# Optimization experiments

Measured on AMD Instinct MI355X. Metric: run time of the kernel, lower is better.

## Reference

```python
import jax, jax.numpy as jnp
import numpy as np

N = 4096
F_IN = 512
F_OUT = 64
H = 8
ALPHA = 0.2
NEG_BIG = -9e15


def setup_inputs() -> dict:
    key = jax.random.key(0)
    ks = jax.random.split(key, 7)
    h = jax.random.normal(ks[0], (N, F_IN), dtype=jnp.float32)
    mask = jax.random.randint(ks[1], (N, N), 0, 2, dtype=jnp.int32)
    # per-head linear W: weight [H, F_IN, F_OUT], bias [H, F_OUT] (xavier-ish scale)
    w_scale = 1.414 * np.sqrt(6.0 / (F_IN + F_OUT))
    W = jax.random.uniform(ks[2], (H, F_IN, F_OUT), dtype=jnp.float32, minval=-w_scale, maxval=w_scale)
    bW = jnp.zeros((H, F_OUT), dtype=jnp.float32)
    # attention linear A: [2*F_OUT, 1] split into a_l (acts on Wh_i) and a_r (acts on Wh_j)
    a_scale = 1.414 * np.sqrt(6.0 / (2 * F_OUT + 1))
    a_l = jax.random.uniform(ks[3], (H, F_OUT), dtype=jnp.float32, minval=-a_scale, maxval=a_scale)
    a_r = jax.random.uniform(ks[4], (H, F_OUT), dtype=jnp.float32, minval=-a_scale, maxval=a_scale)
    bA = jnp.zeros((H,), dtype=jnp.float32)
    return {"h": h, "mask": mask, "W": W, "bW": bW, "a_l": a_l, "a_r": a_r, "bA": bA}


def reference(h, mask, W, bW, a_l, a_r, bA):
    # Wh: [H, N, F_OUT]
    Wh = jnp.einsum('ni,hio->hno', h, W) + bW[:, None, :]
    # A([Wh_i ; Wh_j]) decomposed as outer sum: e[h,i,j] = a_l.Wh_i + a_r.Wh_j + bA
    el = jnp.einsum('hno,ho->hn', Wh, a_l)  # [H, N]
    er = jnp.einsum('hno,ho->hn', Wh, a_r)  # [H, N]
    e = el[:, :, None] + er[:, None, :] + bA[:, None, None]  # [H, N, N]
    e = jax.nn.leaky_relu(e, negative_slope=ALPHA)
    e = jnp.where(mask[None] > 0, e, NEG_BIG)
    a = jax.nn.softmax(e, axis=-1)  # softmax over neighbors j (dim=1 in torch)
    # dropout omitted (eval mode / deterministic reference)
    aWh = jnp.einsum('hij,hjo->hio', a, Wh)  # [H, N, F_OUT]
    out = jax.nn.elu(aWh)  # last=False
    # concat heads along feature dim -> [N, H*F_OUT]
    return jnp.transpose(out, (1, 0, 2)).reshape(N, H * F_OUT)
```

## Files before the change

### kernel.cpp

```cpp
#include <hip/hip_runtime.h>
#include <hip/hip_bf16.h>

#define NN 4096
#define FIN 512
#define FOUT 64
#define NH 8
#define ALPHA 0.2f

typedef unsigned int uint;
typedef unsigned short ushort;
typedef unsigned char uchar;
typedef unsigned long long ull;
typedef __attribute__((ext_vector_type(8))) short short8;
typedef __attribute__((ext_vector_type(4))) float floatx4;

__device__ __forceinline__ float bf2f(ushort s) { return __uint_as_float(((uint)s) << 16); }
__device__ __forceinline__ ushort f2bf(float f) {
    uint u = __float_as_uint(f);
    u += 0x7fffu + ((u >> 16) & 1u);
    return (ushort)(u >> 16);
}

__device__ __forceinline__ int detect_bf16(const ushort* __restrict__ hraw) {
    int lane = threadIdx.x & 63;
    float a = fabsf(bf2f(hraw[2 * lane]));
    ull bal = __ballot(a >= 1e-3f && a <= 100.0f);
    return __popcll(bal) >= 32;
}

#define PM_BLKS 8192
#define CV_BLKS 1024
#define TW_BLKS 32

__global__ __launch_bounds__(256) void prep_kernel(
    const int* __restrict__ mask, uchar* __restrict__ mb,
    const void* __restrict__ hraw, ushort* __restrict__ bh,
    const void* __restrict__ Wraw, ushort* __restrict__ WT)
{
    const int b = blockIdx.x, t = threadIdx.x;
    if (b < PM_BLKS) {
        size_t gid = (size_t)b * 256 + t;
        const int* p = mask + gid * 8;
        int4 aa = *(const int4*)p;
        int4 bb = *(const int4*)(p + 4);
        uint by = (uint)(aa.x > 0)        | ((uint)(aa.y > 0) << 1)
                | ((uint)(aa.z > 0) << 2) | ((uint)(aa.w > 0) << 3)
                | ((uint)(bb.x > 0) << 4) | ((uint)(bb.y > 0) << 5)
                | ((uint)(bb.z > 0) << 6) | ((uint)(bb.w > 0) << 7);
        mb[gid] = (uchar)by;
    } else if (b < PM_BLKS + CV_BLKS) {
        int isbf = detect_bf16((const ushort*)hraw);
        size_t e0 = ((size_t)(b - PM_BLKS) * 256 + t) * 8;
        if (isbf) {
            *(uint4*)(bh + e0) = *(const uint4*)((const ushort*)hraw + e0);
        } else {
            const float* s = (const float*)hraw + e0;
            float4 f0 = *(const float4*)s;
            float4 f1 = *(const float4*)(s + 4);
            uint4 o;
            o.x = (uint)f2bf(f0.x) | ((uint)f2bf(f0.y) << 16);
            o.y = (uint)f2bf(f0.z) | ((uint)f2bf(f0.w) << 16);
            o.z = (uint)f2bf(f1.x) | ((uint)f2bf(f1.y) << 16);
            o.w = (uint)f2bf(f1.z) | ((uint)f2bf(f1.w) << 16);
            *(uint4*)(bh + e0) = o;
        }
    } else {
        int isbf = detect_bf16((const ushort*)hraw);
        int b2 = b - PM_BLKS - CV_BLKS;
        int h = b2 >> 2, kq = b2 & 3;
        int o = t & 63, sub = t >> 6;
        int kbase = kq * 128 + sub * 32;
        uint pk[16];
#pragma unroll
        for (int kk = 0; kk < 32; kk += 2) {
            float v0, v1;
            size_t s0 = ((size_t)h * FIN + kbase + kk) * FOUT + o;
            size_t s1 = s0 + FOUT;
            if (isbf) { v0 = bf2f(((const ushort*)Wraw)[s0]); v1 = bf2f(((const ushort*)Wraw)[s1]); }
            else      { v0 = ((const float*)Wraw)[s0];        v1 = ((const float*)Wraw)[s1]; }
            pk[kk >> 1] = (uint)f2bf(v0) | ((uint)f2bf(v1) << 16);
        }
        ushort* dst = WT + ((size_t)h * FOUT + o) * FIN + kbase;
#pragma unroll
        for (int q = 0; q < 4; q++)
            *(uint4*)(dst + q * 8) = make_uint4(pk[q*4], pk[q*4+1], pk[q*4+2], pk[q*4+3]);
    }
}

__global__ __launch_bounds__(256) void khv_kernel(const float* __restrict__ er,
                                                  float* __restrict__ Kh,
                                                  float* __restrict__ vt,
                                                  float* __restrict__ zt) {
    __shared__ float red[256];
    int h = blockIdx.x >> 3, sl = blockIdx.x & 7, t = threadIdx.x;
    float m = -3.0e38f;
    for (int j = t; j < NN; j += 256) m = fmaxf(m, er[(size_t)h * NN + j]);
    red[t] = m;
    __syncthreads();
    for (int s = 128; s >= 1; s >>= 1) {
        if (t < s) red[t] = fmaxf(red[t], red[t + s]);
        __syncthreads();
    }
    float kh = red[0];
    if (t == 0 && sl == 0) Kh[h] = kh;
    int j = sl * 512 + t;
#pragma unroll
    for (int q = 0; q < 2; q++, j += 256) {
        float d = er[(size_t)h * NN + j] - kh;
        vt[(size_t)h * NN + j] = __expf(d);
        zt[(size_t)h * NN + j] = __expf(ALPHA * d);
    }
}

__global__ __launch_bounds__(256) void wh_kernel(
    const ushort* __restrict__ hmat, const ushort* __restrict__ WT,
    const void* __restrict__ bWr, const void* __restrict__ alr,
    const void* __restrict__ arr, const void* __restrict__ bAr,
    const ushort* __restrict__ hraw,
    ushort* __restrict__ WhT, float* __restrict__ el, float* __restrict__ er)
{
    __shared__ __align__(16) ushort sT[64][72];
    const int t = threadIdx.x, lane = t & 63, wid = t >> 6;
    const int head = blockIdx.y, rbase = blockIdx.x * 64;
    const int lm = lane & 15, lq = lane >> 4;

    floatx4 C[4];
#pragma unroll
    for (int cg = 0; cg < 4; cg++) C[cg] = (floatx4){0.f, 0.f, 0.f, 0.f};

    const ushort* Ap = hmat + (size_t)(rbase + wid * 16 + lm) * FIN + lq * 8;
    const ushort* Bp = WT + (size_t)head * FOUT * FIN + (size_t)lm * FIN + lq * 8;

#pragma unroll
    for (int kc = 0; kc < 16; kc++) {
        short8 a = *(const short8*)(Ap + kc * 32);
#pragma unroll
        for (int cg = 0; cg < 4; cg++) {
            short8 b = *(const short8*)(Bp + (size_t)cg * 16 * FIN + kc * 32);
            C[cg] = __builtin_amdgcn_mfma_f32_16x16x32_bf16(a, b, C[cg], 0, 0, 0);
        }
    }

    const int isbf = detect_bf16(hraw);
    float bA = isbf ? bf2f(((const ushort*)bAr)[head]) : ((const float*)bAr)[head];
    float pel[4] = {0.f, 0.f, 0.f, 0.f}, per[4] = {0.f, 0.f, 0.f, 0.f};
#pragma unroll
    for (int cg = 0; cg < 4; cg++) {
        int o = head * FOUT + cg * 16 + lm;
        float bw = isbf ? bf2f(((const ushort*)bWr)[o]) : ((const float*)bWr)[o];
        float av = isbf ? bf2f(((const ushort*)alr)[o]) : ((const float*)alr)[o];
        float rv = isbf ? bf2f(((const ushort*)arr)[o]) : ((const float*)arr)[o];
        ushort pk[4];
#pragma unroll
        for (int r = 0; r < 4; r++) {
            float v = C[cg][r] + bw;
            pel[r] += v * av;
            per[r] += v * rv;
            pk[r] = f2bf(v);
        }
        ushort4 p4; p4.x = pk[0]; p4.y = pk[1]; p4.z = pk[2]; p4.w = pk[3];
        *(ushort4*)(&sT[cg * 16 + lm][wid * 16 + lq * 4]) = p4;
    }
#pragma unroll
    for (int off = 1; off < 16; off <<= 1) {
#pragma unroll
        for (int r = 0; r < 4; r++) {
            pel[r] += __shfl_xor(pel[r], off);
            per[r] += __shfl_xor(per[r], off);
        }
    }
    if (lm == 0) {
#pragma unroll
        for (int r = 0; r < 4; r++) {
            int row = rbase + wid * 16 + lq * 4 + r;
            el[(size_t)head * NN + row] = pel[r];
            er[(size_t)head * NN + row] = per[r] + bA;
        }
    }
    __syncthreads();
    {
        int o = t >> 2, ch = t & 3;
        uint4 v0 = *(const uint4*)(&sT[o][ch * 16]);
        uint4 v1 = *(const uint4*)(&sT[o][ch * 16 + 8]);
        ushort* d = WhT + ((size_t)head * FOUT + o) * NN + rbase + ch * 16;
        *(uint4*)d = v0;
        *(uint4*)(d + 8) = v1;
    }
}

__device__ __forceinline__ uint ppair(float v0, float v1, float z0, float z1,
                                      uint m2, float ui, float wi) {
    float p0 = fmaxf(ui * v0, wi * z0);
    float p1 = fmaxf(ui * v1, wi * z1);
    uint k0 = (uint)0 - (m2 & 1u);
    uint k1 = (uint)0 - ((m2 >> 1) & 1u);
    p0 = __uint_as_float(__float_as_uint(p0) & k0);
    p1 = __uint_as_float(__float_as_uint(p1) & k1);
    __hip_bfloat162 r = __float22bfloat162_rn(make_float2(p0, p1));
    return *(uint*)&r;
}

__device__ __forceinline__ short8 pgen8(float4 va, float4 vb, float4 za, float4 zb,
                                        uint mby, float ui, float wi) {
    union { uint4 u; short8 s; } c;
    c.u.x = ppair(va.x, va.y, za.x, za.y, mby,      ui, wi);
    c.u.y = ppair(va.z, va.w, za.z, za.w, mby >> 2, ui, wi);
    c.u.z = ppair(vb.x, vb.y, zb.x, zb.y, mby >> 4, ui, wi);
    c.u.w = ppair(vb.z, vb.w, zb.z, zb.w, mby >> 6, ui, wi);
    return c.s;
}

#define VZLOAD(S, j0) do {                                      \
    v##S##a = *(const float4*)(gvt + (j0) + sh8);               \
    v##S##b = *(const float4*)(gvt + (j0) + sh8 + 4);           \
    v##S##c = *(const float4*)(gvt + (j0) + 32 + sh8);          \
    v##S##d = *(const float4*)(gvt + (j0) + 32 + sh8 + 4);      \
    z##S##a = *(const float4*)(gzt + (j0) + sh8);               \
    z##S##b = *(const float4*)(gzt + (j0) + sh8 + 4);           \
    z##S##c = *(const float4*)(gzt + (j0) + 32 + sh8);          \
    z##S##d = *(const float4*)(gzt + (j0) + 32 + sh8 + 4);      \
} while (0)

__global__ __launch_bounds__(256, 2) void attn_kernel(
    const uchar* __restrict__ mb,
    const ushort* __restrict__ WhT,
    const float* __restrict__ el, const float* __restrict__ Kh,
    const float* __restrict__ vt, const float* __restrict__ zt,
    const ushort* __restrict__ hraw,
    void* __restrict__ outv)
{
    __shared__ __align__(16) ushort sB[2][64 * 72];

    const int t = threadIdx.x, lane = t & 63, wid = t >> 6;
    const int b = blockIdx.x;
    const int head = b & 7;
    const int ibase = (b >> 3) * 64;
    const int lm = lane & 15, lq = lane >> 4;
    const int sh8 = lq * 8;

    const float kh = Kh[head];
    const int row = ibase + wid * 16 + lm;
    const float x = el[(size_t)head * NN + row] + kh;
    const float Mi = fmaxf(x, ALPHA * x);
    const float ui = __expf(x - Mi);
    const float wi = __expf(ALPHA * x - Mi);

    const int so = t >> 2;
    const int sc = (t & 3) * 16;
    const ushort* gB = WhT + ((size_t)head * FOUT + so) * NN + sc;
    const float* gvt = vt + (size_t)head * NN;
    const float* gzt = zt + (size_t)head * NN;
    const uchar* mrow = mb + (size_t)row * 512;

    uint4 rr0, rr1;
    uint2 mk_s;

    auto gload = [&](int j0) {
        rr0 = *(const uint4*)(gB + j0);
        rr1 = *(const uint4*)(gB + j0 + 8);
        mk_s = *(const uint2*)(mrow + (j0 >> 3));
    };
    auto lwrite = [&](int buf) {
        ushort* d = &sB[buf][so * 72 + sc];
        *(uint4*)(d)     = rr0;
        *(uint4*)(d + 8) = rr1;
    };

    float4 v0a, v0b, v0c, v0d, z0a, z0b, z0c, z0d;
    float4 v1a, v1b, v1c, v1d, z1a, z1b, z1c, z1d;

    const short8 ones = {0x3F80, 0x3F80, 0x3F80, 0x3F80, 0x3F80, 0x3F80, 0x3F80, 0x3F80};
    floatx4 Z = {0.f, 0.f, 0.f, 0.f};
    floatx4 C0 = Z, C1 = Z, C2 = Z, C3 = Z, Cd = Z;

    auto compute = [&](int buf, uint2 mk,
                       float4 va, float4 vb, float4 vc, float4 vd,
                       float4 za, float4 zb, float4 zc, float4 zd) {
        uint m0 = (mk.x >> sh8) & 0xFFu;
        uint m1 = (mk.y >> sh8) & 0xFFu;
        short8 a0 = pgen8(va, vb, za, zb, m0, ui, wi);
        short8 a1 = pgen8(vc, vd, zc, zd, m1, ui, wi);
        const ushort* base = &sB[buf][0];
        short8 b00 = *(const short8*)(base + (0  + lm) * 72 + sh8);
        short8 b10 = *(const short8*)(base + (16 + lm) * 72 + sh8);
        short8 b20 = *(const short8*)(base + (32 + lm) * 72 + sh8);
        short8 b30 = *(const short8*)(base + (48 + lm) * 72 + sh8);
        Cd = __builtin_amdgcn_mfma_f32_16x16x32_bf16(a0, ones, Cd, 0, 0, 0);
        C0 = __builtin_amdgcn_mfma_f32_16x16x32_bf16(a0, b00, C0, 0, 0, 0);
        C1 = __builtin_amdgcn_mfma_f32_16x16x32_bf16(a0, b10, C1, 0, 0, 0);
        C2 = __builtin_amdgcn_mfma_f32_16x16x32_bf16(a0, b20, C2, 0, 0, 0);
        C3 = __builtin_amdgcn_mfma_f32_16x16x32_bf16(a0, b30, C3, 0, 0, 0);
        short8 b01 = *(const short8*)(base + (0  + lm) * 72 + 32 + sh8);
        short8 b11 = *(const short8*)(base + (16 + lm) * 72 + 32 + sh8);
        short8 b21 = *(const short8*)(base + (32 + lm) * 72 + 32 + sh8);
        short8 b31 = *(const short8*)(base + (48 + lm) * 72 + 32 + sh8);
        Cd = __builtin_amdgcn_mfma_f32_16x16x32_bf16(a1, ones, Cd, 0, 0, 0);
        C0 = __builtin_amdgcn_mfma_f32_16x16x32_bf16(a1, b01, C0, 0, 0, 0);
        C1 = __builtin_amdgcn_mfma_f32_16x16x32_bf16(a1, b11, C1, 0, 0, 0);
        C2 = __builtin_amdgcn_mfma_f32_16x16x32_bf16(a1, b21, C2, 0, 0, 0);
        C3 = __builtin_amdgcn_mfma_f32_16x16x32_bf16(a1, b31, C3, 0, 0, 0);
    };

    uint2 mk0, mk1;
    gload(0);
    lwrite(0);
    mk0 = mk_s;
    gload(64);
    VZLOAD(0, 0);
    __syncthreads();

    for (int it = 0; it < 64; it += 2) {
        lwrite(1);
        mk1 = mk_s;
        gload(((it + 2) & 63) * 64);
        VZLOAD(1, (it + 1) * 64);
        compute(0, mk0, v0a, v0b, v0c, v0d, z0a, z0b, z0c, z0d);
        __syncthreads();
        lwrite(0);
        mk0 = mk_s;
        gload(((it + 3) & 63) * 64);
        VZLOAD(0, ((it + 2) & 63) * 64);
        compute(1, mk1, v1a, v1b, v1c, v1d, z1a, z1b, z1c, z1d);
        __syncthreads();
    }

    const int isbf = detect_bf16(hraw);
#pragma unroll
    for (int r = 0; r < 4; r++) {
        int orow = ibase + wid * 16 + lq * 4 + r;
        float inv = 1.f / Cd[r];
        float x0 = C0[r] * inv; x0 = (x0 > 0.f) ? x0 : __expf(x0) - 1.f;
        float x1 = C1[r] * inv; x1 = (x1 > 0.f) ? x1 : __expf(x1) - 1.f;
        float x2 = C2[r] * inv; x2 = (x2 > 0.f) ? x2 : __expf(x2) - 1.f;
        float x3 = C3[r] * inv; x3 = (x3 > 0.f) ? x3 : __expf(x3) - 1.f;
        size_t base = (size_t)orow * (NH * FOUT) + head * FOUT + lm;
        if (isbf) {
            ushort* o = (ushort*)outv;
            o[base + 0]  = f2bf(x0);
            o[base + 16] = f2bf(x1);
            o[base + 32] = f2bf(x2);
            o[base + 48] = f2bf(x3);
        } else {
            float* o = (float*)outv;
            o[base + 0]  = x0;
            o[base + 16] = x1;
            o[base + 32] = x2;
            o[base + 48] = x3;
        }
    }
}

extern "C" void kernel_launch(void* const* d_in, const int* in_sizes, int n_in,
                              void* d_out, int out_size, void* d_ws, size_t ws_size,
                              hipStream_t stream)
{
    const void* hraw = d_in[0];
    const int*  mask = (const int*)d_in[1];
    const void* Wraw = d_in[2];
    const void* bWr  = d_in[3];
    const void* alr  = d_in[4];
    const void* arr  = d_in[5];
    const void* bAr  = d_in[6];

    char* w = (char*)d_ws;
    ushort* bh   = (ushort*)w;                  w += (size_t)NN * FIN * 2;
    ushort* WT   = (ushort*)w;                  w += (size_t)NH * FOUT * FIN * 2;
    ushort* WhT  = (ushort*)w;                  w += (size_t)NH * FOUT * NN * 2;
    float*  el   = (float*)w;                   w += (size_t)NH * NN * 4;
    float*  er   = (float*)w;                   w += (size_t)NH * NN * 4;
    float*  Kh   = (float*)w;                   w += 64;
    float*  vt   = (float*)w;                   w += (size_t)NH * NN * 4;
    float*  zt   = (float*)w;                   w += (size_t)NH * NN * 4;
    uchar*  mb   = (uchar*)w;                   w += (size_t)NN * 512;

    prep_kernel<<<PM_BLKS + CV_BLKS + TW_BLKS, 256, 0, stream>>>(
        mask, mb, hraw, bh, Wraw, WT);
    wh_kernel<<<dim3(NN / 64, NH), 256, 0, stream>>>(bh, WT, bWr, alr, arr, bAr,
                                                     (const ushort*)hraw, WhT, el, er);
    khv_kernel<<<64, 256, 0, stream>>>(er, Kh, vt, zt);
    attn_kernel<<<NN / 64 * NH, 256, 0, stream>>>(mb, WhT, el, Kh, vt, zt,
                                                  (const ushort*)hraw, d_out);
}
```

Measured before the change: 190.1 us.

## Split neighbor loop across two wave groups per block and reduce through LDS

The attention block grows to 512 threads made of two groups of four waves. Each group handles half of the neighbor range (j), using its own double-buffered LDS tile of Wh. At the end, group 1 writes its partial accumulators and softmax denominators to LDS, and group 0 adds them before normalizing and applying ELU. The aim is to double resident waves per CU and halve each wave's serial loop. In exchange it adds an LDS reduction step and tighter launch bounds, which may force fewer registers and cause spills.

```diff
diff --git a/kernel.cpp b/kernel.cpp
--- a/kernel.cpp
+++ b/kernel.cpp
@@ -221,7 +221,7 @@
     z##S##d = *(const float4*)(gzt + (j0) + 32 + sh8 + 4);      \
 } while (0)
 
-__global__ __launch_bounds__(256, 2) void attn_kernel(
+__global__ __launch_bounds__(512, 4) void attn_kernel(
     const uchar* __restrict__ mb,
     const ushort* __restrict__ WhT,
     const float* __restrict__ el, const float* __restrict__ Kh,
@@ -229,9 +229,11 @@
     const ushort* __restrict__ hraw,
     void* __restrict__ outv)
 {
-    __shared__ __align__(16) ushort sB[2][64 * 72];
+    __shared__ __align__(16) ushort sB[2][2][64 * 72];
 
     const int t = threadIdx.x, lane = t & 63, wid = t >> 6;
+    const int g  = wid >> 2;
+    const int wv = wid & 3;
     const int b = blockIdx.x;
     const int head = b & 7;
     const int ibase = (b >> 3) * 64;
@@ -239,18 +241,19 @@
     const int sh8 = lq * 8;
 
     const float kh = Kh[head];
-    const int row = ibase + wid * 16 + lm;
+    const int row = ibase + wv * 16 + lm;
     const float x = el[(size_t)head * NN + row] + kh;
     const float Mi = fmaxf(x, ALPHA * x);
     const float ui = __expf(x - Mi);
     const float wi = __expf(ALPHA * x - Mi);
 
-    const int so = t >> 2;
-    const int sc = (t & 3) * 16;
-    const ushort* gB = WhT + ((size_t)head * FOUT + so) * NN + sc;
-    const float* gvt = vt + (size_t)head * NN;
-    const float* gzt = zt + (size_t)head * NN;
-    const uchar* mrow = mb + (size_t)row * 512;
+    const int st = t & 255;
+    const int so = st >> 2;
+    const int sc = (st & 3) * 16;
+    const ushort* gB = WhT + ((size_t)head * FOUT + so) * NN + g * 2048 + sc;
+    const float* gvt = vt + (size_t)head * NN + g * 2048;
+    const float* gzt = zt + (size_t)head * NN + g * 2048;
+    const uchar* mrow = mb + (size_t)row * 512 + g * 256;
 
     uint4 rr0, rr1;
     uint2 mk_s;
@@ -261,7 +264,7 @@
         mk_s = *(const uint2*)(mrow + (j0 >> 3));
     };
     auto lwrite = [&](int buf) {
-        ushort* d = &sB[buf][so * 72 + sc];
+        ushort* d = &sB[g][buf][so * 72 + sc];
         *(uint4*)(d)     = rr0;
         *(uint4*)(d + 8) = rr1;
     };
@@ -280,7 +283,7 @@
         uint m1 = (mk.y >> sh8) & 0xFFu;
         short8 a0 = pgen8(va, vb, za, zb, m0, ui, wi);
         short8 a1 = pgen8(vc, vd, zc, zd, m1, ui, wi);
-        const ushort* base = &sB[buf][0];
+        const ushort* base = &sB[g][buf][0];
         short8 b00 = *(const short8*)(base + (0  + lm) * 72 + sh8);
         short8 b10 = *(const short8*)(base + (16 + lm) * 72 + sh8);
         short8 b20 = *(const short8*)(base + (32 + lm) * 72 + sh8);
@@ -309,43 +312,66 @@
     VZLOAD(0, 0);
     __syncthreads();
 
-    for (int it = 0; it < 64; it += 2) {
+    for (int it = 0; it < 32; it += 2) {
         lwrite(1);
         mk1 = mk_s;
-        gload(((it + 2) & 63) * 64);
+        gload(((it + 2) & 31) * 64);
         VZLOAD(1, (it + 1) * 64);
         compute(0, mk0, v0a, v0b, v0c, v0d, z0a, z0b, z0c, z0d);
         __syncthreads();
         lwrite(0);
         mk0 = mk_s;
-        gload(((it + 3) & 63) * 64);
-        VZLOAD(0, ((it + 2) & 63) * 64);
+        gload(((it + 3) & 31) * 64);
+        VZLOAD(0, ((it + 2) & 31) * 64);
         compute(1, mk1, v1a, v1b, v1c, v1d, z1a, z1b, z1c, z1d);
         __syncthreads();
     }
 
-    const int isbf = detect_bf16(hraw);
-#pragma unroll
-    for (int r = 0; r < 4; r++) {
-        int orow = ibase + wid * 16 + lq * 4 + r;
-        float inv = 1.f / Cd[r];
-        float x0 = C0[r] * inv; x0 = (x0 > 0.f) ? x0 : __expf(x0) - 1.f;
-        float x1 = C1[r] * inv; x1 = (x1 > 0.f) ? x1 : __expf(x1) - 1.f;
-        float x2 = C2[r] * inv; x2 = (x2 > 0.f) ? x2 : __expf(x2) - 1.f;
-        float x3 = C3[r] * inv; x3 = (x3 > 0.f) ? x3 : __expf(x3) - 1.f;
-        size_t base = (size_t)orow * (NH * FOUT) + head * FOUT + lm;
-        if (isbf) {
-            ushort* o = (ushort*)outv;
-            o[base + 0]  = f2bf(x0);
-            o[base + 16] = f2bf(x1);
-            o[base + 32] = f2bf(x2);
-            o[base + 48] = f2bf(x3);
-        } else {
-            float* o = (float*)outv;
-            o[base + 0]  = x0;
-            o[base + 16] = x1;
-            o[base + 32] = x2;
-            o[base + 48] = x3;
+    float* mg = (float*)&sB[0][0][0];
+    const int mi = (wv * 64 + lane) * 21;
+    if (g == 1) {
+#pragma unroll
+        for (int r = 0; r < 4; r++) {
+            mg[mi + r]      = C0[r];
+            mg[mi + 4 + r]  = C1[r];
+            mg[mi + 8 + r]  = C2[r];
+            mg[mi + 12 + r] = C3[r];
+            mg[mi + 16 + r] = Cd[r];
+        }
+    }
+    __syncthreads();
+    if (g == 0) {
+#pragma unroll
+        for (int r = 0; r < 4; r++) {
+            C0[r] += mg[mi + r];
+            C1[r] += mg[mi + 4 + r];
+            C2[r] += mg[mi + 8 + r];
+            C3[r] += mg[mi + 12 + r];
+            Cd[r] += mg[mi + 16 + r];
+        }
+        const int isbf = detect_bf16(hraw);
+#pragma unroll
+        for (int r = 0; r < 4; r++) {
+            int orow = ibase + wv * 16 + lq * 4 + r;
+            float inv = 1.f / Cd[r];
+            float x0 = C0[r] * inv; x0 = (x0 > 0.f) ? x0 : __expf(x0) - 1.f;
+            float x1 = C1[r] * inv; x1 = (x1 > 0.f) ? x1 : __expf(x1) - 1.f;
+            float x2 = C2[r] * inv; x2 = (x2 > 0.f) ? x2 : __expf(x2) - 1.f;
+            float x3 = C3[r] * inv; x3 = (x3 > 0.f) ? x3 : __expf(x3) - 1.f;
+            size_t base = (size_t)orow * (NH * FOUT) + head * FOUT + lm;
+            if (isbf) {
+                ushort* o = (ushort*)outv;
+                o[base + 0]  = f2bf(x0);
+                o[base + 16] = f2bf(x1);
+                o[base + 32] = f2bf(x2);
+                o[base + 48] = f2bf(x3);
+            } else {
+                float* o = (float*)outv;
+                o[base + 0]  = x0;
+                o[base + 16] = x1;
+                o[base + 32] = x2;
+                o[base + 48] = x3;
+            }
         }
     }
 }
@@ -378,6 +404,6 @@
     wh_kernel<<<dim3(NN / 64, NH), 256, 0, stream>>>(bh, WT, bWr, alr, arr, bAr,
                                                      (const ushort*)hraw, WhT, el, er);
     khv_kernel<<<64, 256, 0, stream>>>(er, Kh, vt, zt);
-    attn_kernel<<<NN / 64 * NH, 256, 0, stream>>>(mb, WhT, el, Kh, vt, zt,
+    attn_kernel<<<NN / 64 * NH, 512, 0, stream>>>(mb, WhT, el, Kh, vt, zt,
                                                   (const ushort*)hraw, d_out);
 }
```

Result: no change. 193.8 us (+1.9%).

## Switch attention probabilities and Wh to fp16 with packed-half probability generation

Applied to the files above, without the earlier changes.

Stores the vt/zt exponent tables and WhT as fp16 instead of fp32/bf16, and generates the attention probabilities with packed v_pk_mul/v_pk_max f16 instructions and bitmask ANDs instead of per-element fp32 math and bf16 conversion. The MFMAs switch from bf16 to f16, and the row factors are prescaled by 4096 to stay in fp16 range. The goal is to halve vt/zt load traffic and register use and to cut VALU work in the inner loop. Empty asm keep-alives pin prefetched registers to the intended pipeline order. The risk is fp16 overflow or underflow in the scaled probabilities and accumulations.

```diff
diff --git a/kernel.cpp b/kernel.cpp
--- a/kernel.cpp
+++ b/kernel.cpp
@@ -1,24 +1,32 @@
 #include <hip/hip_runtime.h>
 #include <hip/hip_bf16.h>
+#include <hip/hip_fp16.h>
 
 #define NN 4096
 #define FIN 512
 #define FOUT 64
 #define NH 8
 #define ALPHA 0.2f
+#define PSCALE 4096.0f
 
 typedef unsigned int uint;
 typedef unsigned short ushort;
 typedef unsigned char uchar;
 typedef unsigned long long ull;
 typedef __attribute__((ext_vector_type(8))) short short8;
+typedef __attribute__((ext_vector_type(8))) _Float16 half8;
 typedef __attribute__((ext_vector_type(4))) float floatx4;
+typedef __attribute__((ext_vector_type(4))) uint uintx4;
+typedef __attribute__((ext_vector_type(2))) uint uintx2;
 
 __device__ __forceinline__ float bf2f(ushort s) { return __uint_as_float(((uint)s) << 16); }
 __device__ __forceinline__ ushort f2bf(float f) {
     uint u = __float_as_uint(f);
     u += 0x7fffu + ((u >> 16) & 1u);
     return (ushort)(u >> 16);
+}
+__device__ __forceinline__ ushort f2h(float f) {
+    return __half_as_ushort(__float2half_rn(f));
 }
 
 __device__ __forceinline__ int detect_bf16(const ushort* __restrict__ hraw) {
@@ -89,8 +97,8 @@
 
 __global__ __launch_bounds__(256) void khv_kernel(const float* __restrict__ er,
                                                   float* __restrict__ Kh,
-                                                  float* __restrict__ vt,
-                                                  float* __restrict__ zt) {
+                                                  ushort* __restrict__ vt,
+                                                  ushort* __restrict__ zt) {
     __shared__ float red[256];
     int h = blockIdx.x >> 3, sl = blockIdx.x & 7, t = threadIdx.x;
     float m = -3.0e38f;
@@ -107,8 +115,8 @@
 #pragma unroll
     for (int q = 0; q < 2; q++, j += 256) {
         float d = er[(size_t)h * NN + j] - kh;
-        vt[(size_t)h * NN + j] = __expf(d);
-        zt[(size_t)h * NN + j] = __expf(ALPHA * d);
+        vt[(size_t)h * NN + j] = f2h(__expf(d));
+        zt[(size_t)h * NN + j] = f2h(__expf(ALPHA * d));
     }
 }
 
@@ -156,7 +164,7 @@
             float v = C[cg][r] + bw;
             pel[r] += v * av;
             per[r] += v * rv;
-            pk[r] = f2bf(v);
+            pk[r] = f2h(v);
         }
         ushort4 p4; p4.x = pk[0]; p4.y = pk[1]; p4.z = pk[2]; p4.w = pk[3];
         *(ushort4*)(&sT[cg * 16 + lm][wid * 16 + lq * 4]) = p4;
@@ -188,44 +196,40 @@
     }
 }
 
-__device__ __forceinline__ uint ppair(float v0, float v1, float z0, float z1,
-                                      uint m2, float ui, float wi) {
-    float p0 = fmaxf(ui * v0, wi * z0);
-    float p1 = fmaxf(ui * v1, wi * z1);
-    uint k0 = (uint)0 - (m2 & 1u);
-    uint k1 = (uint)0 - ((m2 >> 1) & 1u);
-    p0 = __uint_as_float(__float_as_uint(p0) & k0);
-    p1 = __uint_as_float(__float_as_uint(p1) & k1);
-    __hip_bfloat162 r = __float22bfloat162_rn(make_float2(p0, p1));
-    return *(uint*)&r;
-}
-
-__device__ __forceinline__ short8 pgen8(float4 va, float4 vb, float4 za, float4 zb,
-                                        uint mby, float ui, float wi) {
-    union { uint4 u; short8 s; } c;
-    c.u.x = ppair(va.x, va.y, za.x, za.y, mby,      ui, wi);
-    c.u.y = ppair(va.z, va.w, za.z, za.w, mby >> 2, ui, wi);
-    c.u.z = ppair(vb.x, vb.y, zb.x, zb.y, mby >> 4, ui, wi);
-    c.u.w = ppair(vb.z, vb.w, zb.z, zb.w, mby >> 6, ui, wi);
-    return c.s;
-}
-
-#define VZLOAD(S, j0) do {                                      \
-    v##S##a = *(const float4*)(gvt + (j0) + sh8);               \
-    v##S##b = *(const float4*)(gvt + (j0) + sh8 + 4);           \
-    v##S##c = *(const float4*)(gvt + (j0) + 32 + sh8);          \
-    v##S##d = *(const float4*)(gvt + (j0) + 32 + sh8 + 4);      \
-    z##S##a = *(const float4*)(gzt + (j0) + sh8);               \
-    z##S##b = *(const float4*)(gzt + (j0) + sh8 + 4);           \
-    z##S##c = *(const float4*)(gzt + (j0) + 32 + sh8);          \
-    z##S##d = *(const float4*)(gzt + (j0) + 32 + sh8 + 4);      \
+__device__ __forceinline__ uint pkmul(uint a, uint b) {
+    uint d; asm("v_pk_mul_f16 %0,%1,%2" : "=v"(d) : "v"(a), "v"(b)); return d;
+}
+__device__ __forceinline__ uint pkmax(uint a, uint b) {
+    uint d; asm("v_pk_max_f16 %0,%1,%2" : "=v"(d) : "v"(a), "v"(b)); return d;
+}
+__device__ __forceinline__ uint pmask2(uint a) {
+    uint b = a & 3u;
+    return ((b | (b << 15)) & 0x10001u) * 0xFFFFu;
+}
+__device__ __forceinline__ half8 pgen8h(uintx4 vv, uintx4 zz, uint mby,
+                                        uint uip, uint wip) {
+    union { uintx4 u; half8 h; } c;
+    c.u.x = pkmax(pkmul(uip, vv.x), pkmul(wip, zz.x)) & pmask2(mby);
+    c.u.y = pkmax(pkmul(uip, vv.y), pkmul(wip, zz.y)) & pmask2(mby >> 2);
+    c.u.z = pkmax(pkmul(uip, vv.z), pkmul(wip, zz.z)) & pmask2(mby >> 4);
+    c.u.w = pkmax(pkmul(uip, vv.w), pkmul(wip, zz.w)) & pmask2(mby >> 6);
+    return c.h;
+}
+
+#define KEEP(x) asm volatile("" : "+v"(x))
+
+#define VZLOAD(S, j0) do {                                   \
+    v##S##a = *(const uintx4*)(gvt + (j0) + sh8);            \
+    v##S##b = *(const uintx4*)(gvt + (j0) + 32 + sh8);       \
+    z##S##a = *(const uintx4*)(gzt + (j0) + sh8);            \
+    z##S##b = *(const uintx4*)(gzt + (j0) + 32 + sh8);       \
 } while (0)
 
 __global__ __launch_bounds__(256, 2) void attn_kernel(
     const uchar* __restrict__ mb,
     const ushort* __restrict__ WhT,
     const float* __restrict__ el, const float* __restrict__ Kh,
-    const float* __restrict__ vt, const float* __restrict__ zt,
+    const ushort* __restrict__ vt, const ushort* __restrict__ zt,
     const ushort* __restrict__ hraw,
     void* __restrict__ outv)
 {
@@ -242,71 +246,73 @@
     const int row = ibase + wid * 16 + lm;
     const float x = el[(size_t)head * NN + row] + kh;
     const float Mi = fmaxf(x, ALPHA * x);
-    const float ui = __expf(x - Mi);
-    const float wi = __expf(ALPHA * x - Mi);
+    const uint uip = (uint)f2h(PSCALE * __expf(x - Mi)) * 0x10001u;
+    const uint wip = (uint)f2h(PSCALE * __expf(ALPHA * x - Mi)) * 0x10001u;
 
     const int so = t >> 2;
     const int sc = (t & 3) * 16;
     const ushort* gB = WhT + ((size_t)head * FOUT + so) * NN + sc;
-    const float* gvt = vt + (size_t)head * NN;
-    const float* gzt = zt + (size_t)head * NN;
+    const ushort* gvt = vt + (size_t)head * NN;
+    const ushort* gzt = zt + (size_t)head * NN;
     const uchar* mrow = mb + (size_t)row * 512;
 
-    uint4 rr0, rr1;
-    uint2 mk_s;
+    uintx4 rr0, rr1;
+    uintx2 mk_s;
 
     auto gload = [&](int j0) {
-        rr0 = *(const uint4*)(gB + j0);
-        rr1 = *(const uint4*)(gB + j0 + 8);
-        mk_s = *(const uint2*)(mrow + (j0 >> 3));
+        rr0 = *(const uintx4*)(gB + j0);
+        rr1 = *(const uintx4*)(gB + j0 + 8);
+        mk_s = *(const uintx2*)(mrow + (j0 >> 3));
     };
     auto lwrite = [&](int buf) {
         ushort* d = &sB[buf][so * 72 + sc];
-        *(uint4*)(d)     = rr0;
-        *(uint4*)(d + 8) = rr1;
+        *(uintx4*)(d)     = rr0;
+        *(uintx4*)(d + 8) = rr1;
     };
 
-    float4 v0a, v0b, v0c, v0d, z0a, z0b, z0c, z0d;
-    float4 v1a, v1b, v1c, v1d, z1a, z1b, z1c, z1d;
-
-    const short8 ones = {0x3F80, 0x3F80, 0x3F80, 0x3F80, 0x3F80, 0x3F80, 0x3F80, 0x3F80};
+    uintx4 v0a, v0b, z0a, z0b;
+    uintx4 v1a, v1b, z1a, z1b;
+
+    const half8 onesh = {(_Float16)1.f, (_Float16)1.f, (_Float16)1.f, (_Float16)1.f,
+                         (_Float16)1.f, (_Float16)1.f, (_Float16)1.f, (_Float16)1.f};
     floatx4 Z = {0.f, 0.f, 0.f, 0.f};
     floatx4 C0 = Z, C1 = Z, C2 = Z, C3 = Z, Cd = Z;
 
-    auto compute = [&](int buf, uint2 mk,
-                       float4 va, float4 vb, float4 vc, float4 vd,
-                       float4 za, float4 zb, float4 zc, float4 zd) {
-        uint m0 = (mk.x >> sh8) & 0xFFu;
-        uint m1 = (mk.y >> sh8) & 0xFFu;
-        short8 a0 = pgen8(va, vb, za, zb, m0, ui, wi);
-        short8 a1 = pgen8(vc, vd, zc, zd, m1, ui, wi);
+    auto compute = [&](int buf, uintx2 mk,
+                       uintx4 vA, uintx4 vB, uintx4 zA, uintx4 zB) {
+        uint m0 = mk.x >> sh8;
+        uint m1 = mk.y >> sh8;
+        half8 a0 = pgen8h(vA, zA, m0, uip, wip);
+        half8 a1 = pgen8h(vB, zB, m1, uip, wip);
         const ushort* base = &sB[buf][0];
-        short8 b00 = *(const short8*)(base + (0  + lm) * 72 + sh8);
-        short8 b10 = *(const short8*)(base + (16 + lm) * 72 + sh8);
-        short8 b20 = *(const short8*)(base + (32 + lm) * 72 + sh8);
-        short8 b30 = *(const short8*)(base + (48 + lm) * 72 + sh8);
-        Cd = __builtin_amdgcn_mfma_f32_16x16x32_bf16(a0, ones, Cd, 0, 0, 0);
-        C0 = __builtin_amdgcn_mfma_f32_16x16x32_bf16(a0, b00, C0, 0, 0, 0);
-        C1 = __builtin_amdgcn_mfma_f32_16x16x32_bf16(a0, b10, C1, 0, 0, 0);
-        C2 = __builtin_amdgcn_mfma_f32_16x16x32_bf16(a0, b20, C2, 0, 0, 0);
-        C3 = __builtin_amdgcn_mfma_f32_16x16x32_bf16(a0, b30, C3, 0, 0, 0);
-        short8 b01 = *(const short8*)(base + (0  + lm) * 72 + 32 + sh8);
-        short8 b11 = *(const short8*)(base + (16 + lm) * 72 + 32 + sh8);
-        short8 b21 = *(const short8*)(base + (32 + lm) * 72 + 32 + sh8);
-        short8 b31 = *(const short8*)(base + (48 + lm) * 72 + 32 + sh8);
-        Cd = __builtin_amdgcn_mfma_f32_16x16x32_bf16(a1, ones, Cd, 0, 0, 0);
-        C0 = __builtin_amdgcn_mfma_f32_16x16x32_bf16(a1, b01, C0, 0, 0, 0);
-        C1 = __builtin_amdgcn_mfma_f32_16x16x32_bf16(a1, b11, C1, 0, 0, 0);
-        C2 = __builtin_amdgcn_mfma_f32_16x16x32_bf16(a1, b21, C2, 0, 0, 0);
-        C3 = __builtin_amdgcn_mfma_f32_16x16x32_bf16(a1, b31, C3, 0, 0, 0);
+        half8 b00 = *(const half8*)(base + (0  + lm) * 72 + sh8);
+        half8 b10 = *(const half8*)(base + (16 + lm) * 72 + sh8);
+        half8 b20 = *(const half8*)(base + (32 + lm) * 72 + sh8);
+        half8 b30 = *(const half8*)(base + (48 + lm) * 72 + sh8);
+        Cd = __builtin_amdgcn_mfma_f32_16x16x32_f16(a0, onesh, Cd, 0, 0, 0);
+        C0 = __builtin_amdgcn_mfma_f32_16x16x32_f16(a0, b00, C0, 0, 0, 0);
+        C1 = __builtin_amdgcn_mfma_f32_16x16x32_f16(a0, b10, C1, 0, 0, 0);
+        C2 = __builtin_amdgcn_mfma_f32_16x16x32_f16(a0, b20, C2, 0, 0, 0);
+        C3 = __builtin_amdgcn_mfma_f32_16x16x32_f16(a0, b30, C3, 0, 0, 0);
+        half8 b01 = *(const half8*)(base + (0  + lm) * 72 + 32 + sh8);
+        half8 b11 = *(const half8*)(base + (16 + lm) * 72 + 32 + sh8);
+        half8 b21 = *(const half8*)(base + (32 + lm) * 72 + 32 + sh8);
+        half8 b31 = *(const half8*)(base + (48 + lm) * 72 + 32 + sh8);
+        Cd = __builtin_amdgcn_mfma_f32_16x16x32_f16(a1, onesh, Cd, 0, 0, 0);
+        C0 = __builtin_amdgcn_mfma_f32_16x16x32_f16(a1, b01, C0, 0, 0, 0);
+        C1 = __builtin_amdgcn_mfma_f32_16x16x32_f16(a1, b11, C1, 0, 0, 0);
+        C2 = __builtin_amdgcn_mfma_f32_16x16x32_f16(a1, b21, C2, 0, 0, 0);
+        C3 = __builtin_amdgcn_mfma_f32_16x16x32_f16(a1, b31, C3, 0, 0, 0);
     };
 
-    uint2 mk0, mk1;
+    uintx2 mk0, mk1;
     gload(0);
     lwrite(0);
     mk0 = mk_s;
     gload(64);
     VZLOAD(0, 0);
+    KEEP(rr0); KEEP(rr1); KEEP(mk_s);
+    KEEP(v0a); KEEP(v0b); KEEP(z0a); KEEP(z0b);
     __syncthreads();
 
     for (int it = 0; it < 64; it += 2) {
@@ -314,13 +320,17 @@
         mk1 = mk_s;
         gload(((it + 2) & 63) * 64);
         VZLOAD(1, (it + 1) * 64);
-        compute(0, mk0, v0a, v0b, v0c, v0d, z0a, z0b, z0c, z0d);
+        compute(0, mk0, v0a, v0b, z0a, z0b);
+        KEEP(v1a); KEEP(v1b); KEEP(z1a); KEEP(z1b);
+        KEEP(rr0); KEEP(rr1); KEEP(mk_s);
         __syncthreads();
         lwrite(0);
         mk0 = mk_s;
         gload(((it + 3) & 63) * 64);
         VZLOAD(0, ((it + 2) & 63) * 64);
-        compute(1, mk1, v1a, v1b, v1c, v1d, z1a, z1b, z1c, z1d);
+        compute(1, mk1, v1a, v1b, z1a, z1b);
+        KEEP(v0a); KEEP(v0b); KEEP(z0a); KEEP(z0b);
+        KEEP(rr0); KEEP(rr1); KEEP(mk_s);
         __syncthreads();
     }
 
@@ -369,8 +379,8 @@
     float*  el   = (float*)w;                   w += (size_t)NH * NN * 4;
     float*  er   = (float*)w;                   w += (size_t)NH * NN * 4;
     float*  Kh   = (float*)w;                   w += 64;
-    float*  vt   = (float*)w;                   w += (size_t)NH * NN * 4;
-    float*  zt   = (float*)w;                   w += (size_t)NH * NN * 4;
+    ushort* vt   = (ushort*)w;                  w += (size_t)NH * NN * 4;
+    ushort* zt   = (ushort*)w;                  w += (size_t)NH * NN * 4;
     uchar*  mb   = (uchar*)w;                   w += (size_t)NN * 512;
 
     prep_kernel<<<PM_BLKS + CV_BLKS + TW_BLKS, 256, 0, stream>>>(
```

Result: slower. 195.9 us (+3.0%).
